# Kernel tuning notes

Hardware: AMD Instinct MI355X
Metric: run time of the kernel (lower is better)

## Reference

```python
import jax, jax.numpy as jnp
import numpy as np

B, N, F, T, KCHEB, O = 8, 1024, 64, 12, 3, 64

def setup_inputs() -> dict:
    key = jax.random.key(0)
    k1, k2, k3, k4 = jax.random.split(key, 4)
    graph_signal = jax.random.normal(k1, (B, N, F, T), dtype=jnp.float32)
    spatial_attention = jax.random.uniform(k2, (B, N, N), dtype=jnp.float32)
    # Chebyshev polynomials of scaled Laplacian, scaled to keep magnitudes sane
    cheb = jax.random.normal(k3, (KCHEB, N, N), dtype=jnp.float32) / np.float32(np.sqrt(N))
    # theta: (K, F, num_of_filters), glorot-ish scale
    theta = jax.random.normal(k4, (KCHEB, F, O), dtype=jnp.float32) / np.float32(np.sqrt(F))
    return {"graph_signal": graph_signal, "spatial_attention": spatial_attention,
            "cheb": cheb, "theta": theta}

def reference(graph_signal, spatial_attention, cheb, theta):
    # Original loops over t and k computing:
    #   rhs[b,n,f] = sum_m (T_k[m,n] * att[b,m,n]) * x[b,m,f,t]   (transposed batch_dot)
    #   out[b,n,o,t] += rhs @ theta[k]
    # Vectorized over k, t in one pass.
    Ak = cheb[:, None, :, :] * spatial_attention[None]          # (K,B,N,N) = T_k * attention
    rhs = jnp.einsum('kbmn,bmft->kbnft', Ak, graph_signal)      # T_k_with_at^T @ x for all t
    out = jnp.einsum('kbnft,kfo->bnot', rhs, theta)             # sum over k and f
    return jax.nn.relu(out)                                     # (B, N, O, T)
```

## Files before the change

### kernel.cpp

```cpp
#include <hip/hip_runtime.h>
#include <stdint.h>

#define NB 8
#define NN 1024
#define NF 64
#define NT 12
#define NK 3
#define NO 64
#define NQ 768
#define KKC 3072

typedef __attribute__((ext_vector_type(8))) short bf16x8;
typedef __attribute__((ext_vector_type(4))) float f32x4;

typedef const unsigned int __attribute__((address_space(1)))* gas1_t;
typedef unsigned int __attribute__((address_space(3)))* las3_t;

__device__ __forceinline__ void gload_lds16(const void* g, void* l) {
  __builtin_amdgcn_global_load_lds((gas1_t)g, (las3_t)l, 16, 0, 0);
}

__device__ __forceinline__ unsigned short f2bf(float f) {
  union { float f; unsigned int u; } v; v.f = f;
  unsigned int u = v.u;
  unsigned int r = (u + 0x7FFFu + ((u >> 16) & 1u)) >> 16;
  return (unsigned short)r;
}

__global__ void k0_thetaT(const float* __restrict__ theta, unsigned short* __restrict__ thT) {
  int i = blockIdx.x * 256 + threadIdx.x;
  if (i >= NK * NO * NF) return;
  int f = i & 63, o = (i >> 6) & 63, k = i >> 12;
  thT[i] = f2bf(theta[(k * NF + f) * NO + o]);
}

__global__ __launch_bounds__(256) void k1_A2(const float* __restrict__ cheb,
                                             const float* __restrict__ att,
                                             unsigned short* __restrict__ A2) {
  __shared__ float att_s[64][65];
  __shared__ float cheb_s[64][65];
  const int n0 = blockIdx.x * 64;
  const int m0 = blockIdx.y * 64;
  const int b  = blockIdx.z;
  const int tid = threadIdx.x;
  const int r4 = tid >> 4;
  const int c  = tid & 15;

#pragma unroll
  for (int p = 0; p < 4; ++p) {
    int r = r4 + p * 16;
    const float4 v = *(const float4*)(att + ((size_t)(b * NN + m0 + r)) * NN + n0 + c * 4);
    att_s[r][c * 4 + 0] = v.x; att_s[r][c * 4 + 1] = v.y;
    att_s[r][c * 4 + 2] = v.z; att_s[r][c * 4 + 3] = v.w;
  }
  for (int k = 0; k < NK; ++k) {
#pragma unroll
    for (int p = 0; p < 4; ++p) {
      int r = r4 + p * 16;
      const float4 v = *(const float4*)(cheb + ((size_t)(k * NN + m0 + r)) * NN + n0 + c * 4);
      cheb_s[r][c * 4 + 0] = v.x; cheb_s[r][c * 4 + 1] = v.y;
      cheb_s[r][c * 4 + 2] = v.z; cheb_s[r][c * 4 + 3] = v.w;
    }
    __syncthreads();
#pragma unroll
    for (int p = 0; p < 8; ++p) {
      int e  = p * 256 + tid;
      int jn = e >> 5;
      int q  = e & 31;
      float f0 = att_s[2 * q][jn]     * cheb_s[2 * q][jn];
      float f1 = att_s[2 * q + 1][jn] * cheb_s[2 * q + 1][jn];
      unsigned int pk = (unsigned int)f2bf(f0) | ((unsigned int)f2bf(f1) << 16);
      size_t el = ((size_t)(b * NN + n0 + jn)) * KKC + k * NN + m0 + 2 * q;
      *(unsigned int*)(A2 + el) = pk;
    }
    __syncthreads();
  }
}

__global__ __launch_bounds__(256) void k2_xT(const float* __restrict__ x,
                                             unsigned short* __restrict__ xT) {
  __shared__ unsigned int lds[12][16][32];
  const int m0 = blockIdx.x * 16;
  const int b  = blockIdx.y;
  const int tid = threadIdx.x;
  const float* xb = x + ((size_t)(b * NN + m0)) * (NF * NT);

#pragma unroll
  for (int u0 = 0; u0 < 2; ++u0) {
    const int u  = u0 * 256 + tid;
    const int ml = u >> 5;
    const int fp = u & 31;
    const float* src = xb + ((size_t)ml * NF + fp * 2) * NT;
    float v[24];
#pragma unroll
    for (int i = 0; i < 6; ++i)
      *(float4*)(v + i * 4) = *(const float4*)(src + i * 4);
#pragma unroll
    for (int t = 0; t < 12; ++t) {
      unsigned int pk = (unsigned int)f2bf(v[t]) | ((unsigned int)f2bf(v[t + 12]) << 16);
      lds[t][ml][fp] = pk;
    }
  }
  __syncthreads();

#pragma unroll
  for (int it = 0; it < 12; ++it) {
    const int g = it * 256 + tid;
    const int t = g >> 8;
    const int r = g & 255;
    const int m = r >> 4;
    const int f4 = r & 15;
    uint2 u = *(const uint2*)&lds[t][m][2 * f4];
    size_t el = (((size_t)(b * NT + t) * NN) + m0 + m) * NF + f4 * 4;
    *(uint2*)(void*)(xT + el) = u;
  }
}

__global__ __launch_bounds__(256) void k3_Y(const unsigned short* __restrict__ xT,
                                            const unsigned short* __restrict__ thT,
                                            unsigned short* __restrict__ Y) {
  __shared__ unsigned short Xs[256 * 64];
  const int mc = blockIdx.x;
  const int t  = blockIdx.y;
  const int b  = blockIdx.z;
  const int tid = threadIdx.x;
  const int w = tid >> 6, l = tid & 63;
  const int lrow = l & 15, lk = l >> 4;

  const unsigned short* xbase = xT + ((size_t)(b * NT + t)) * NN * NF + (size_t)(mc * 256) * NF;

#pragma unroll
  for (int it = 0; it < 8; ++it) {
    const int idx = it * 256 + tid;
    const int r   = idx >> 3;
    const int c16 = (idx & 7) ^ (r & 7);
    gload_lds16(xbase + (size_t)r * NF + c16 * 8, Xs + (size_t)idx * 8);
  }
  __syncthreads();

  bf16x8 af[2][4];
#pragma unroll
  for (int ks = 0; ks < 2; ++ks)
#pragma unroll
    for (int mi = 0; mi < 4; ++mi) {
      const int row = w * 64 + mi * 16 + lrow;
      const int sw = (row * 128 + ks * 64 + lk * 16) ^ ((row & 7) << 4);
      af[ks][mi] = *(const bf16x8*)((const char*)Xs + sw);
    }

  for (int k = 0; k < NK; ++k) {
    const unsigned short* tb = thT + (size_t)k * NO * NF;
    f32x4 acc[4][4] = {};
#pragma unroll
    for (int ks = 0; ks < 2; ++ks) {
      bf16x8 bb[4];
#pragma unroll
      for (int oj = 0; oj < 4; ++oj)
        bb[oj] = *(const bf16x8*)(tb + (size_t)(oj * 16 + lrow) * NF + ks * 32 + lk * 8);
#pragma unroll
      for (int mi = 0; mi < 4; ++mi)
#pragma unroll
        for (int oj = 0; oj < 4; ++oj)
          acc[mi][oj] = __builtin_amdgcn_mfma_f32_16x16x32_bf16(af[ks][mi], bb[oj], acc[mi][oj], 0, 0, 0);
    }
#pragma unroll
    for (int mi = 0; mi < 4; ++mi) {
#pragma unroll
      for (int oj = 0; oj < 4; ++oj) {
        const int o  = oj * 16 + lrow;
        const int mg = mc * 256 + w * 64 + mi * 16 + lk * 4;
        uint2 u;
        u.x = (unsigned int)f2bf(acc[mi][oj][0]) | ((unsigned int)f2bf(acc[mi][oj][1]) << 16);
        u.y = (unsigned int)f2bf(acc[mi][oj][2]) | ((unsigned int)f2bf(acc[mi][oj][3]) << 16);
        size_t el = ((size_t)(b * NQ + o * NT + t)) * KKC + k * NN + mg;
        *(uint2*)(void*)(Y + el) = u;
      }
    }
  }
}

__global__ __launch_bounds__(256) void k4_main(const unsigned short* __restrict__ A2,
                                               const unsigned short* __restrict__ Y,
                                               float* __restrict__ out) {
  __shared__ unsigned short Asl0[64 * 64],  Asl1[64 * 64];
  __shared__ unsigned short Bsl0[128 * 64], Bsl1[128 * 64];
  const int tid = threadIdx.x;
  const int w = tid >> 6, l = tid & 63;
  const int lrow = l & 15, lk = l >> 4;
  const int wm = w >> 1, wq = w & 1;

  const int lin = (blockIdx.x & 7) * 96 + (blockIdx.x >> 3);
  const int b   = lin / 96;
  const int rem = lin % 96;
  const int bn  = rem / 6;
  const int bq  = rem % 6;

  const unsigned short* Abase = A2 + ((size_t)(b * NN + bn * 64)) * KKC;
  const unsigned short* Bbase = Y  + ((size_t)(b * NQ + bq * 128)) * KKC;

  f32x4 acc[2][4] = {};

  auto STAGE = [&](unsigned short* Ad, unsigned short* Bd, int kt) {
    const int kb = kt * 64;
#pragma unroll
    for (int it = 0; it < 2; ++it) {
      const int idx = it * 256 + tid;
      const int r   = idx >> 3;
      const int c16 = (idx & 7) ^ (r & 7);
      gload_lds16(Abase + (size_t)r * KKC + kb + c16 * 8, Ad + (size_t)idx * 8);
    }
#pragma unroll
    for (int it = 0; it < 4; ++it) {
      const int idx = it * 256 + tid;
      const int r   = idx >> 3;
      const int c16 = (idx & 7) ^ (r & 7);
      gload_lds16(Bbase + (size_t)r * KKC + kb + c16 * 8, Bd + (size_t)idx * 8);
    }
  };

  auto COMPUTE = [&](const unsigned short* As, const unsigned short* Bs) {
#pragma unroll
    for (int kss = 0; kss < 2; ++kss) {
      bf16x8 af[2], bfr[4];
#pragma unroll
      for (int mi = 0; mi < 2; ++mi) {
        const int row = wm * 32 + mi * 16 + lrow;
        const int sw = (row * 128 + kss * 64 + lk * 16) ^ ((row & 7) << 4);
        af[mi] = *(const bf16x8*)((const char*)As + sw);
      }
#pragma unroll
      for (int nj = 0; nj < 4; ++nj) {
        const int row = wq * 64 + nj * 16 + lrow;
        const int sw = (row * 128 + kss * 64 + lk * 16) ^ ((row & 7) << 4);
        bfr[nj] = *(const bf16x8*)((const char*)Bs + sw);
      }
#pragma unroll
      for (int mi = 0; mi < 2; ++mi)
#pragma unroll
        for (int nj = 0; nj < 4; ++nj)
          acc[mi][nj] = __builtin_amdgcn_mfma_f32_16x16x32_bf16(af[mi], bfr[nj], acc[mi][nj], 0, 0, 0);
    }
  };

  STAGE(Asl0, Bsl0, 0);
  __syncthreads();
  for (int kt = 0; kt < KKC / 64; kt += 2) {
    STAGE(Asl1, Bsl1, kt + 1);
    COMPUTE(Asl0, Bsl0);
    __syncthreads();
    if (kt + 2 < KKC / 64) STAGE(Asl0, Bsl0, kt + 2);
    COMPUTE(Asl1, Bsl1);
    __syncthreads();
  }

  const int nb0 = bn * 64 + wm * 32;
  const int qb0 = bq * 128 + wq * 64;
#pragma unroll
  for (int mi = 0; mi < 2; ++mi) {
#pragma unroll
    for (int nj = 0; nj < 4; ++nj) {
      const int q = qb0 + nj * 16 + lrow;
#pragma unroll
      for (int j = 0; j < 4; ++j) {
        const int n = nb0 + mi * 16 + lk * 4 + j;
        float v = acc[mi][nj][j];
        out[((size_t)(b * NN + n)) * NQ + q] = v > 0.f ? v : 0.f;
      }
    }
  }
}

extern "C" void kernel_launch(void* const* d_in, const int* in_sizes, int n_in,
                              void* d_out, int out_size, void* d_ws, size_t ws_size,
                              hipStream_t stream) {
  const float* x     = (const float*)d_in[0];
  const float* att   = (const float*)d_in[1];
  const float* cheb  = (const float*)d_in[2];
  const float* theta = (const float*)d_in[3];
  float* out = (float*)d_out;

  char* ws = (char*)d_ws;
  unsigned short* A2  = (unsigned short*)(ws);
  unsigned short* xT  = (unsigned short*)(ws + 50331648);
  unsigned short* Y   = (unsigned short*)(ws + 62914560);
  unsigned short* thT = (unsigned short*)(ws + 100663296);

  k0_thetaT<<<48, 256, 0, stream>>>(theta, thT);
  k1_A2<<<dim3(16, 16, 8), 256, 0, stream>>>(cheb, att, A2);
  k2_xT<<<dim3(64, 8), 256, 0, stream>>>(x, xT);
  k3_Y<<<dim3(4, 12, 8), 256, 0, stream>>>(xT, thT, Y);
  k4_main<<<768, 256, 0, stream>>>(A2, Y, out);
}
```

Measured before the change: 105.2 us.

## Replace double-buffered K pipeline with single buffer and wider K tile

The main GEMM kernel drops its two-stage LDS double buffering (64-wide K tiles) and uses a single buffer holding 128-wide K tiles, with the XOR swizzle widened from 8 to 16 chunks. Each iteration loads a tile, syncs, computes four k-substeps, then syncs again. This halves the number of loop iterations and barriers per K element and keeps the same LDS footprint, but it gives up overlap between global-to-LDS loads and MFMA compute, so each tile's load latency is exposed unless other resident blocks hide it.

```diff
diff --git a/kernel.cpp b/kernel.cpp
--- a/kernel.cpp
+++ b/kernel.cpp
@@ -182,8 +182,8 @@
 __global__ __launch_bounds__(256) void k4_main(const unsigned short* __restrict__ A2,
                                                const unsigned short* __restrict__ Y,
                                                float* __restrict__ out) {
-  __shared__ unsigned short Asl0[64 * 64],  Asl1[64 * 64];
-  __shared__ unsigned short Bsl0[128 * 64], Bsl1[128 * 64];
+  __shared__ unsigned short Asl[64 * 128];
+  __shared__ unsigned short Bsl[128 * 128];
   const int tid = threadIdx.x;
   const int w = tid >> 6, l = tid & 63;
   const int lrow = l & 15, lk = l >> 4;
@@ -200,39 +200,37 @@
 
   f32x4 acc[2][4] = {};
 
-  auto STAGE = [&](unsigned short* Ad, unsigned short* Bd, int kt) {
-    const int kb = kt * 64;
-#pragma unroll
-    for (int it = 0; it < 2; ++it) {
-      const int idx = it * 256 + tid;
-      const int r   = idx >> 3;
-      const int c16 = (idx & 7) ^ (r & 7);
-      gload_lds16(Abase + (size_t)r * KKC + kb + c16 * 8, Ad + (size_t)idx * 8);
-    }
+  for (int kt = 0; kt < KKC / 128; ++kt) {
+    const int kb = kt * 128;
 #pragma unroll
     for (int it = 0; it < 4; ++it) {
       const int idx = it * 256 + tid;
-      const int r   = idx >> 3;
-      const int c16 = (idx & 7) ^ (r & 7);
-      gload_lds16(Bbase + (size_t)r * KKC + kb + c16 * 8, Bd + (size_t)idx * 8);
-    }
-  };
-
-  auto COMPUTE = [&](const unsigned short* As, const unsigned short* Bs) {
-#pragma unroll
-    for (int kss = 0; kss < 2; ++kss) {
+      const int r   = idx >> 4;
+      const int c16 = (idx & 15) ^ (r & 15);
+      gload_lds16(Abase + (size_t)r * KKC + kb + c16 * 8, Asl + (size_t)idx * 8);
+    }
+#pragma unroll
+    for (int it = 0; it < 8; ++it) {
+      const int idx = it * 256 + tid;
+      const int r   = idx >> 4;
+      const int c16 = (idx & 15) ^ (r & 15);
+      gload_lds16(Bbase + (size_t)r * KKC + kb + c16 * 8, Bsl + (size_t)idx * 8);
+    }
+    __syncthreads();
+#pragma unroll
+    for (int ks = 0; ks < 4; ++ks) {
       bf16x8 af[2], bfr[4];
 #pragma unroll
       for (int mi = 0; mi < 2; ++mi) {
         const int row = wm * 32 + mi * 16 + lrow;
-        const int sw = (row * 128 + kss * 64 + lk * 16) ^ ((row & 7) << 4);
-        af[mi] = *(const bf16x8*)((const char*)As + sw);
+        const int sw = (row * 256 + ks * 64 + lk * 16) ^ ((row & 15) << 4);
+        af[mi] = *(const bf16x8*)((const char*)Asl + sw);
       }
 #pragma unroll
       for (int nj = 0; nj < 4; ++nj) {
         const int row = wq * 64 + nj * 16 + lrow;
-        const int sw = (row * 128 + kss * 64 + lk * 16) ^ ((row & 7) << 4);
-        bfr[nj] = *(const bf16x8*)((const char*)Bs + sw);
+        const int sw = (row * 256 + ks * 64 + lk * 16) ^ ((row & 15) << 4);
+        bfr[nj] = *(const bf16x8*)((const char*)Bsl + sw);
       }
 #pragma unroll
       for (int mi = 0; mi < 2; ++mi)
@@ -240,16 +238,6 @@
         for (int nj = 0; nj < 4; ++nj)
           acc[mi][nj] = __builtin_amdgcn_mfma_f32_16x16x32_bf16(af[mi], bfr[nj], acc[mi][nj], 0, 0, 0);
     }
-  };
-
-  STAGE(Asl0, Bsl0, 0);
-  __syncthreads();
-  for (int kt = 0; kt < KKC / 64; kt += 2) {
-    STAGE(Asl1, Bsl1, kt + 1);
-    COMPUTE(Asl0, Bsl0);
-    __syncthreads();
-    if (kt + 2 < KKC / 64) STAGE(Asl0, Bsl0, kt + 2);
-    COMPUTE(Asl1, Bsl1);
     __syncthreads();
   }
 
```

Measured after the change: 105.0 us. Within noise of the previous version (-0.2%).
